# Optimization experiments

Measured on AMD Instinct MI355X. Metric: run time of the kernel, lower is better.

The kernel has to match this reference:

```python
import jax, jax.numpy as jnp
import numpy as np

B, S, D_IN, D_OUT = 4, 2048, 1024, 1024

def setup_inputs() -> dict:
    key = jax.random.key(0)
    kx, kq, kk, kv = jax.random.split(key, 4)
    sc = 1.0 / np.sqrt(D_IN)
    x = jax.random.normal(kx, (B, S, D_IN), dtype=jnp.float32)
    Wq = jax.random.normal(kq, (D_IN, D_OUT), dtype=jnp.float32) * sc
    Wk = jax.random.normal(kk, (D_IN, D_OUT), dtype=jnp.float32) * sc
    Wv = jax.random.normal(kv, (D_IN, D_OUT), dtype=jnp.float32) * sc
    return {"x": x, "Wq": Wq, "Wk": Wk, "Wv": Wv}

def reference(x, Wq, Wk, Wv):
    # x: [B,S,Din]; projections to [B,S,Dout]
    q = jnp.einsum('bsd,de->bse', x, Wq)
    k = jnp.einsum('bsd,de->bse', x, Wk)
    v = jnp.einsum('bsd,de->bse', x, Wv)
    scale = 1.0 / jnp.sqrt(jnp.asarray(q.shape[-1], q.dtype))
    scores = jnp.einsum('bqe,bke->bqk', q, k) * scale  # [B,S,S]
    causal = jnp.tril(jnp.ones((scores.shape[-2], scores.shape[-1]), dtype=bool))
    scores = jnp.where(causal, scores, -jnp.inf)
    attn = jax.nn.softmax(scores, axis=-1)
    # dropout p=0.0 -> identity
    return jnp.einsum('bqk,bke->bqe', attn, v)
```

## Files before the change

### kernel.cpp

```cpp
#include <hip/hip_runtime.h>

#define SEQ 2048
#define DIM 1024

typedef __attribute__((ext_vector_type(8))) __bf16 bf16x8;
typedef __attribute__((ext_vector_type(4))) float f32x4;

typedef __attribute__((address_space(1))) unsigned char gu8_t;
typedef __attribute__((address_space(3))) unsigned char lu8_t;

__device__ __forceinline__ void async_copy16(const void* g, void* l) {
  __builtin_amdgcn_global_load_lds((gu8_t*)g, (lu8_t*)l, 16, 0, 0);
}

__device__ __forceinline__ ushort f2bf(float f) {
  union { float f; unsigned u; } v;
  v.f = f;
  unsigned r = v.u + 0x7FFFu + ((v.u >> 16) & 1u);
  return (ushort)(r >> 16);
}

__global__ void prep(const void* __restrict__ xin, const void* __restrict__ w0,
                     const void* __restrict__ w1, const void* __restrict__ w2,
                     ushort* __restrict__ xb, ushort* __restrict__ wt,
                     int* __restrict__ flag, float* __restrict__ lsum) {
  __shared__ ushort tile[64][68];
  __shared__ int redi[4];
  const int bid = blockIdx.x;
  const int t = threadIdx.x;

  const unsigned* words = (const unsigned*)xin;
  int hits = 0;
#pragma unroll
  for (int i = 0; i < 4; i++) {
    const unsigned wv = words[t * 4 + i];
    const unsigned b = (wv >> 8) & 0x7Fu;
    hits += (b >= 0x3Bu && b <= 0x42u) ? 1 : 0;
  }
#pragma unroll
  for (int o = 32; o > 0; o >>= 1) hits += __shfl_xor(hits, o, 64);
  if ((t & 63) == 0) redi[t >> 6] = hits;
  __syncthreads();
  const int bf = (redi[0] + redi[1] + redi[2] + redi[3] > 512) ? 1 : 0;

  if (bid >= 4864) {
    reinterpret_cast<float4*>(lsum)[(bid - 4864) * 256 + t] =
        make_float4(0.f, 0.f, 0.f, 0.f);
    if (bid == 4864 && t == 0) *flag = bf;
    return;
  }

  if (bid < 4096) {
    const int i = bid * 256 + t;
    if (bf) {
      reinterpret_cast<uint4*>(xb)[i] =
          reinterpret_cast<const uint4*>(xin)[i];
    } else {
      const float4* f = reinterpret_cast<const float4*>(xin);
      const float4 a = f[2 * i], b = f[2 * i + 1];
      ushort4 lo, hi;
      lo.x = f2bf(a.x); lo.y = f2bf(a.y); lo.z = f2bf(a.z); lo.w = f2bf(a.w);
      hi.x = f2bf(b.x); hi.y = f2bf(b.y); hi.z = f2bf(b.z); hi.w = f2bf(b.w);
      reinterpret_cast<ushort4*>(xb)[2 * i] = lo;
      reinterpret_cast<ushort4*>(xb)[2 * i + 1] = hi;
    }
    return;
  }

  const int rem = bid - 4096;
  const int z = rem >> 8;
  const int within = rem & 255;
  const int c0 = (within & 15) * 64, r0 = (within >> 4) * 64;
  const void* in = (z == 0) ? w0 : (z == 1) ? w1 : w2;
  ushort* op = wt + (size_t)z * 1024 * 1024;

  if (bf) {
    const ushort* ip = (const ushort*)in;
#pragma unroll
    for (int i = 0; i < 4; i++) {
      const int lin = i * 256 + t;
      const int r = lin >> 4, c4 = (lin & 15) << 2;
      const ushort4 v = *reinterpret_cast<const ushort4*>(
          ip + (size_t)(r0 + r) * 1024 + c0 + c4);
      tile[r][c4 + 0] = v.x; tile[r][c4 + 1] = v.y;
      tile[r][c4 + 2] = v.z; tile[r][c4 + 3] = v.w;
    }
  } else {
    const float* ip = (const float*)in;
#pragma unroll
    for (int i = 0; i < 4; i++) {
      const int lin = i * 256 + t;
      const int r = lin >> 4, c4 = (lin & 15) << 2;
      const float4 v = *reinterpret_cast<const float4*>(
          ip + (size_t)(r0 + r) * 1024 + c0 + c4);
      tile[r][c4 + 0] = f2bf(v.x); tile[r][c4 + 1] = f2bf(v.y);
      tile[r][c4 + 2] = f2bf(v.z); tile[r][c4 + 3] = f2bf(v.w);
    }
  }
  __syncthreads();
#pragma unroll
  for (int i = 0; i < 4; i++) {
    const int lin = i * 256 + t;
    const int c = lin >> 4, r4 = (lin & 15) << 2;
    ushort4 v;
    v.x = tile[r4 + 0][c]; v.y = tile[r4 + 1][c];
    v.z = tile[r4 + 2][c]; v.w = tile[r4 + 3][c];
    *reinterpret_cast<ushort4*>(op + (size_t)(c0 + c) * 1024 + r0 + r4) = v;
  }
}

template <int EPI>
__global__ __launch_bounds__(512, 2) void gemm8(
    const ushort* __restrict__ P0, const ushort* __restrict__ P1,
    void* __restrict__ Cv, float* __restrict__ lsum) {
  __shared__ ushort sA[2][2][128 * 64];
  __shared__ ushort sB[2][2][128 * 64];

  const ushort* A;
  const ushort* B;
  ushort* C;
  float* ls = nullptr;
  int m0, n0;
  long ldA, ldB, ldC;
  float scale = 1.0f;

  if constexpr (EPI == 0) {
    const int id = blockIdx.x;
    if (id < 256) {
      const int z = id >> 7, r = id & 127;
      m0 = (r >> 2) << 8;
      n0 = (r & 3) << 8;
      A = P0; ldA = 1024;
      B = P1 + (size_t)z * 1024 * 1024; ldB = 1024;
      C = (ushort*)Cv + (size_t)z * 8192 * 1024; ldC = 1024;
      scale = z ? 1.0f : 0.03125f;
    } else {
      const int r = id - 256;
      m0 = (r >> 5) << 8;
      n0 = (r & 31) << 8;
      A = P1 + 2 * 1024 * 1024; ldA = 1024;
      B = P0; ldB = 1024;
      C = (ushort*)Cv + (size_t)16 * 1024 * 1024; ldC = 8192;
    }
  } else {
    const int id = blockIdx.x, z = blockIdx.y;
    int mt = 0;
    while ((mt + 1) * (mt + 2) / 2 <= id) mt++;
    const int nt = id - mt * (mt + 1) / 2;
    m0 = mt << 8;
    n0 = nt << 8;
    A = P0 + (size_t)z * SEQ * DIM; ldA = 1024;
    B = P0 + (size_t)8192 * 1024 + (size_t)z * SEQ * DIM; ldB = 1024;
    C = (ushort*)Cv + (size_t)z * SEQ * SEQ; ldC = 2048;
    ls = lsum + (size_t)z * SEQ;
  }
  const int nT = 16;

  const int tid = threadIdx.x;
  const int lane = tid & 63;
  const int w = tid >> 6;
  const int quad = lane >> 4;
  const int l15 = lane & 15;
  const int ah = w >> 2;
  const int wn = (w & 3) << 6;
  const int bh = wn >> 7;
  const int bo = wn & 64;

  const ushort* aSrc[2][2];
  const ushort* bSrc[2][2];
#pragma unroll
  for (int h = 0; h < 2; h++)
#pragma unroll
    for (int i = 0; i < 2; i++) {
      const int g = i * 512 + tid;
      const int rl = g >> 3;
      const int ck = (g & 7) ^ (rl & 7);
      aSrc[h][i] = A + (size_t)(m0 + h * 128 + rl) * ldA + ck * 8;
      bSrc[h][i] = B + (size_t)(n0 + h * 128 + rl) * ldB + ck * 8;
    }

  auto stageA = [&](int t, int b) {
#pragma unroll
    for (int h = 0; h < 2; h++)
#pragma unroll
      for (int i = 0; i < 2; i++)
        async_copy16(aSrc[h][i] + t * 64, &sA[b][h][(i * 512 + tid) * 8]);
  };
  auto stageB = [&](int t, int b) {
#pragma unroll
    for (int h = 0; h < 2; h++)
#pragma unroll
      for (int i = 0; i < 2; i++)
        async_copy16(bSrc[h][i] + t * 64, &sB[b][h][(i * 512 + tid) * 8]);
  };
  auto rdA = [&](int b, int rbase, int kh) -> bf16x8 {
    const int row = rbase + l15;
    const int ck = ((kh << 2) | quad) ^ (row & 7);
    return *(const bf16x8*)&sA[b][ah][row * 64 + ck * 8];
  };
  auto rdB = [&](int b, int rbase, int kh) -> bf16x8 {
    const int row = rbase + l15;
    const int ck = ((kh << 2) | quad) ^ (row & 7);
    return *(const bf16x8*)&sB[b][bh][row * 64 + ck * 8];
  };

  f32x4 acc[8][4] = {};
  bf16x8 aF[8], bF0[4], bF1[4];

  stageA(0, 0); stageB(0, 0);
  stageA(1, 1); stageB(1, 1);
  asm volatile("s_waitcnt vmcnt(8)" ::: "memory");
  __builtin_amdgcn_s_barrier();

#pragma unroll 1
  for (int t = 0; t < nT; t++) {
    const int b = t & 1;

#pragma unroll
    for (int m = 0; m < 4; m++)
#pragma unroll
      for (int h = 0; h < 2; h++) aF[m * 2 + h] = rdA(b, m * 16, h);
#pragma unroll
    for (int n = 0; n < 2; n++)
#pragma unroll
      for (int h = 0; h < 2; h++) bF0[n * 2 + h] = rdB(b, bo + n * 16, h);
    __builtin_amdgcn_s_barrier();
    __builtin_amdgcn_s_setprio(1);
#pragma unroll
    for (int h = 0; h < 2; h++)
#pragma unroll
      for (int m = 0; m < 4; m++)
#pragma unroll
        for (int n = 0; n < 2; n++)
          acc[m][n] = __builtin_amdgcn_mfma_f32_16x16x32_bf16(
              aF[m * 2 + h], bF0[n * 2 + h], acc[m][n], 0, 0, 0);
    __builtin_amdgcn_s_setprio(0);
    __builtin_amdgcn_s_barrier();

#pragma unroll
    for (int n = 0; n < 2; n++)
#pragma unroll
      for (int h = 0; h < 2; h++)
        bF1[n * 2 + h] = rdB(b, bo + 32 + n * 16, h);
    __builtin_amdgcn_s_barrier();
    __builtin_amdgcn_s_setprio(1);
#pragma unroll
    for (int h = 0; h < 2; h++)
#pragma unroll
      for (int m = 0; m < 4; m++)
#pragma unroll
        for (int n = 0; n < 2; n++)
          acc[m][2 + n] = __builtin_amdgcn_mfma_f32_16x16x32_bf16(
              aF[m * 2 + h], bF1[n * 2 + h], acc[m][2 + n], 0, 0, 0);
    __builtin_amdgcn_s_setprio(0);
    __builtin_amdgcn_s_barrier();

#pragma unroll
    for (int m = 0; m < 4; m++)
#pragma unroll
      for (int h = 0; h < 2; h++) aF[m * 2 + h] = rdA(b, 64 + m * 16, h);
    if (t + 2 < nT) stageB(t + 2, b);
    __builtin_amdgcn_s_barrier();
    __builtin_amdgcn_s_setprio(1);
#pragma unroll
    for (int h = 0; h < 2; h++)
#pragma unroll
      for (int m = 0; m < 4; m++)
#pragma unroll
        for (int n = 0; n < 2; n++)
          acc[4 + m][n] = __builtin_amdgcn_mfma_f32_16x16x32_bf16(
              aF[m * 2 + h], bF0[n * 2 + h], acc[4 + m][n], 0, 0, 0);
    __builtin_amdgcn_s_setprio(0);
    __builtin_amdgcn_s_barrier();

    if (t + 2 < nT) stageA(t + 2, b);
    __builtin_amdgcn_s_setprio(1);
#pragma unroll
    for (int h = 0; h < 2; h++)
#pragma unroll
      for (int m = 0; m < 4; m++)
#pragma unroll
        for (int n = 0; n < 2; n++)
          acc[4 + m][2 + n] = __builtin_amdgcn_mfma_f32_16x16x32_bf16(
              aF[m * 2 + h], bF1[n * 2 + h], acc[4 + m][2 + n], 0, 0, 0);
    __builtin_amdgcn_s_setprio(0);
    if (t + 2 < nT)
      asm volatile("s_waitcnt vmcnt(8)" ::: "memory");
    else
      asm volatile("s_waitcnt vmcnt(0)" ::: "memory");
    __builtin_amdgcn_s_barrier();
  }

  if constexpr (EPI == 0) {
#pragma unroll
    for (int mi = 0; mi < 8; mi++)
#pragma unroll
      for (int ni = 0; ni < 4; ni++)
#pragma unroll
        for (int r = 0; r < 4; r++) {
          const int row = m0 + ah * 128 + mi * 16 + quad * 4 + r;
          const int col = n0 + wn + ni * 16 + l15;
          C[(size_t)row * ldC + col] = f2bf(acc[mi][ni][r] * scale);
        }
  } else {
#pragma unroll
    for (int mi = 0; mi < 8; mi++)
#pragma unroll
      for (int r = 0; r < 4; r++) {
        const int row = m0 + ah * 128 + mi * 16 + quad * 4 + r;
        float partial = 0.0f;
#pragma unroll
        for (int ni = 0; ni < 4; ni++) {
          const int col = n0 + wn + ni * 16 + l15;
          const float ev = (col <= row) ? __expf(acc[mi][ni][r]) : 0.0f;
          C[(size_t)row * ldC + col] = f2bf(ev);
          partial += ev;
        }
#pragma unroll
        for (int o = 1; o < 16; o <<= 1) partial += __shfl_xor(partial, o, 64);
        if (l15 == 0) atomicAdd(&ls[row], partial);
      }
  }
}

template <int EPI, int OUTK, int CK, int SWIZ, int M, int N, int K, long AZ,
          long BZ, long CZ, long BRS>
__global__ __launch_bounds__(256, 4) void gemm_t(
    const ushort* __restrict__ A, const ushort* __restrict__ Bt,
    void* __restrict__ Cv, const int* __restrict__ flag,
    float* __restrict__ lsum, float scale0, float scale1) {
  __shared__ ushort lA[128 * 64];
  __shared__ ushort lB[128 * 64];
  __shared__ float lsh[(EPI == 2) ? 128 : 1];

  constexpr int MT = M / 128;
  const int nT = gridDim.x;
  const int id = blockIdx.y * nT + blockIdx.x;
  const int xcd = id & 7;
  const int loc = id >> 3;
  int nt, mt;
  if constexpr (SWIZ == 1) {
    const int ng = nT >> 3;
    nt = xcd * ng + loc % ng;
    mt = loc / ng;
  } else if constexpr (SWIZ == 2) {
    if (loc <= xcd) { mt = xcd; nt = loc; }
    else { mt = MT - 1 - xcd; nt = loc - xcd - 1; }
  } else if constexpr (SWIZ == 3) {
    nt = xcd;
    mt = loc;
  } else {
    nt = loc % nT;
    mt = xcd + ((loc / nT) << 3);
  }
  const int n0 = nt * 128;
  const int m0 = mt * 128;

  const int z = blockIdx.z;
  const ushort* Ab = A + (size_t)z * AZ;
  const ushort* Bb = Bt + (size_t)z * BZ;

  const int t = threadIdx.x;
  const int lane = t & 63;
  const int w = t >> 6;
  const int wm = (w >> 1) * 64;
  const int wn = (w & 1) * 64;
  const int quad = lane >> 4;
  const int l15 = lane & 15;

  if constexpr (EPI == 2) {
    if (t < 128) lsh[t] = 1.0f / lsum[(size_t)z * M + m0 + t];
  }

  f32x4 acc[4][4] = {};

  const int kEnd = CK ? ((m0 + 128 < K) ? (m0 + 128) : K) : K;

  for (int k0 = 0; k0 < kEnd; k0 += 64) {
    __syncthreads();
#pragma unroll
    for (int g0 = 0; g0 < 1024; g0 += 256) {
      const int g = g0 + t;
      const int r = g >> 3, c = (g & 7) << 3;
      async_copy16(Ab + (size_t)(m0 + r) * K + k0 + c, lA + g * 8);
    }
#pragma unroll
    for (int g0 = 0; g0 < 1024; g0 += 256) {
      const int g = g0 + t;
      const int r = g >> 3, c = (g & 7) << 3;
      async_copy16(Bb + (size_t)(n0 + r) * BRS + k0 + c, lB + g * 8);
    }
    __syncthreads();

#pragma unroll
    for (int h = 0; h < 2; h++) {
      bf16x8 af[4], bfr[4];
#pragma unroll
      for (int mi = 0; mi < 4; mi++)
        af[mi] = *(const bf16x8*)(lA + (wm + mi * 16 + l15) * 64 + h * 32 +
                                  quad * 8);
#pragma unroll
      for (int ni = 0; ni < 4; ni++)
        bfr[ni] = *(const bf16x8*)(lB + (wn + ni * 16 + l15) * 64 + h * 32 +
                                   quad * 8);
#pragma unroll
      for (int mi = 0; mi < 4; mi++)
#pragma unroll
        for (int ni = 0; ni < 4; ni++)
          acc[mi][ni] = __builtin_amdgcn_mfma_f32_16x16x32_bf16(
              af[mi], bfr[ni], acc[mi][ni], 0, 0, 0);
    }
  }

  const size_t zc = (size_t)z * CZ;

  if constexpr (EPI == 1) {
    ushort* C = (ushort*)Cv + zc;
    float* ls = lsum + (size_t)z * M;
#pragma unroll
    for (int mi = 0; mi < 4; mi++)
#pragma unroll
      for (int r = 0; r < 4; r++) {
        const int row = m0 + wm + mi * 16 + quad * 4 + r;
        float partial = 0.0f;
#pragma unroll
        for (int ni = 0; ni < 4; ni++) {
          const int col = n0 + wn + ni * 16 + l15;
          const float ev = (col <= row) ? __expf(acc[mi][ni][r]) : 0.0f;
          C[(size_t)row * N + col] = f2bf(ev);
          partial += ev;
        }
#pragma unroll
        for (int o = 1; o < 16; o <<= 1) partial += __shfl_xor(partial, o, 64);
        if (l15 == 0) atomicAdd(&ls[row], partial);
      }
    return;
  } else {
    const float scale = (z == 0) ? scale0 : scale1;
    const bool storeBf = (OUTK == 1) || (OUTK == 2 && *flag != 0);
#pragma unroll
    for (int mi = 0; mi < 4; mi++)
#pragma unroll
      for (int ni = 0; ni < 4; ni++)
#pragma unroll
        for (int r = 0; r < 4; r++) {
          const int lrow = wm + mi * 16 + quad * 4 + r;
          const int row = m0 + lrow;
          const int col = n0 + wn + ni * 16 + l15;
          const float sc = (EPI == 2) ? lsh[lrow] : scale;
          const float vv = acc[mi][ni][r] * sc;
          if (storeBf) {
            ushort* C = (ushort*)Cv + zc;
            C[(size_t)row * N + col] = f2bf(vv);
          } else {
            float* C = (float*)Cv + zc;
            C[(size_t)row * N + col] = vv;
          }
        }
  }
}

extern "C" void kernel_launch(void* const* d_in, const int* in_sizes, int n_in,
                              void* d_out, int out_size, void* d_ws,
                              size_t ws_size, hipStream_t stream) {
  char* ws = (char*)d_ws;
  const size_t MB = 1024 * 1024;
  int* flag = (int*)ws;
  ushort* wt = (ushort*)(ws + 1 * MB);
  ushort* xb = (ushort*)(ws + 7 * MB);
  ushort* q = (ushort*)(ws + 23 * MB);
  ushort* vt = (ushort*)(ws + 55 * MB);
  ushort* sc = (ushort*)(ws + 71 * MB);
  float* lsum = (float*)(ws + 103 * MB);

  prep<<<dim3(4872), 256, 0, stream>>>(d_in[0], d_in[1], d_in[2], d_in[3], xb,
                                       wt, flag, lsum);

  gemm8<0><<<dim3(384), 512, 0, stream>>>(xb, wt, (void*)q, nullptr);

  gemm8<1><<<dim3(36, 4), 512, 0, stream>>>(q, nullptr, (void*)sc, lsum);

  gemm_t<2, 2, 1, 3, 2048, 1024, 2048, (long)SEQ * SEQ, 2048L,
         (long)SEQ * DIM, 8192L>
      <<<dim3(8, 16, 4), 256, 0, stream>>>(sc, vt, d_out, flag, lsum, 1.0f,
                                           1.0f);
}
```

Baseline: 247.3 us.

## Move V-transpose projection into score kernel launch and coarsen prep blocks

The V^T projection tiles (128 blocks) move out of the QK projection launch and into the causal score-exp launch, which becomes a flat 272-block grid of 144 score tiles plus 128 V tiles. The aim is to fill the idle CUs left by the small triangular score grid and to shorten the projection launch. The prep kernel's x conversion also handles four vectors per thread, cutting its block count. The cost is a mixed-role kernel with per-block branching in the epilogue, and the score blocks' imbalance may now sit alongside the V tiles.

Result: faster. 241.6 us (-2.3%).

```diff
diff --git a/kernel.cpp b/kernel.cpp
--- a/kernel.cpp
+++ b/kernel.cpp
@@ -43,31 +43,34 @@
   __syncthreads();
   const int bf = (redi[0] + redi[1] + redi[2] + redi[3] > 512) ? 1 : 0;
 
-  if (bid >= 4864) {
-    reinterpret_cast<float4*>(lsum)[(bid - 4864) * 256 + t] =
+  if (bid >= 1792) {
+    reinterpret_cast<float4*>(lsum)[(bid - 1792) * 256 + t] =
         make_float4(0.f, 0.f, 0.f, 0.f);
-    if (bid == 4864 && t == 0) *flag = bf;
+    if (bid == 1792 && t == 0) *flag = bf;
     return;
   }
 
-  if (bid < 4096) {
-    const int i = bid * 256 + t;
-    if (bf) {
-      reinterpret_cast<uint4*>(xb)[i] =
-          reinterpret_cast<const uint4*>(xin)[i];
-    } else {
-      const float4* f = reinterpret_cast<const float4*>(xin);
-      const float4 a = f[2 * i], b = f[2 * i + 1];
-      ushort4 lo, hi;
-      lo.x = f2bf(a.x); lo.y = f2bf(a.y); lo.z = f2bf(a.z); lo.w = f2bf(a.w);
-      hi.x = f2bf(b.x); hi.y = f2bf(b.y); hi.z = f2bf(b.z); hi.w = f2bf(b.w);
-      reinterpret_cast<ushort4*>(xb)[2 * i] = lo;
-      reinterpret_cast<ushort4*>(xb)[2 * i + 1] = hi;
+  if (bid < 1024) {
+#pragma unroll
+    for (int j = 0; j < 4; j++) {
+      const int i = bid * 1024 + j * 256 + t;
+      if (bf) {
+        reinterpret_cast<uint4*>(xb)[i] =
+            reinterpret_cast<const uint4*>(xin)[i];
+      } else {
+        const float4* f = reinterpret_cast<const float4*>(xin);
+        const float4 a = f[2 * i], b = f[2 * i + 1];
+        ushort4 lo, hi;
+        lo.x = f2bf(a.x); lo.y = f2bf(a.y); lo.z = f2bf(a.z); lo.w = f2bf(a.w);
+        hi.x = f2bf(b.x); hi.y = f2bf(b.y); hi.z = f2bf(b.z); hi.w = f2bf(b.w);
+        reinterpret_cast<ushort4*>(xb)[2 * i] = lo;
+        reinterpret_cast<ushort4*>(xb)[2 * i + 1] = hi;
+      }
     }
     return;
   }
 
-  const int rem = bid - 4096;
+  const int rem = bid - 1024;
   const int z = rem >> 8;
   const int within = rem & 255;
   const int c0 = (within & 15) * 64, r0 = (within >> 4) * 64;
@@ -109,10 +112,11 @@
   }
 }
 
-template <int EPI>
+template <int MODE>
 __global__ __launch_bounds__(512, 2) void gemm8(
-    const ushort* __restrict__ P0, const ushort* __restrict__ P1,
-    void* __restrict__ Cv, float* __restrict__ lsum) {
+    const ushort* __restrict__ p0, const ushort* __restrict__ p1,
+    const ushort* __restrict__ p2, void* __restrict__ c0,
+    void* __restrict__ c1, float* __restrict__ lsum) {
   __shared__ ushort sA[2][2][128 * 64];
   __shared__ ushort sB[2][2][128 * 64];
 
@@ -123,36 +127,39 @@
   int m0, n0;
   long ldA, ldB, ldC;
   float scale = 1.0f;
-
-  if constexpr (EPI == 0) {
-    const int id = blockIdx.x;
-    if (id < 256) {
-      const int z = id >> 7, r = id & 127;
-      m0 = (r >> 2) << 8;
-      n0 = (r & 3) << 8;
-      A = P0; ldA = 1024;
-      B = P1 + (size_t)z * 1024 * 1024; ldB = 1024;
-      C = (ushort*)Cv + (size_t)z * 8192 * 1024; ldC = 1024;
-      scale = z ? 1.0f : 0.03125f;
+  bool isE = false;
+
+  const int id = blockIdx.x;
+  if constexpr (MODE == 0) {
+    const int z = id >> 7, r = id & 127;
+    m0 = (r >> 2) << 8;
+    n0 = (r & 3) << 8;
+    A = p0; ldA = 1024;
+    B = p1 + (size_t)z * 1024 * 1024; ldB = 1024;
+    C = (ushort*)c0 + (size_t)z * 8192 * 1024; ldC = 1024;
+    scale = z ? 1.0f : 0.03125f;
+  } else {
+    if (id < 144) {
+      isE = true;
+      const int z = id / 36;
+      const int tri = id % 36;
+      int mt = 0;
+      while ((mt + 1) * (mt + 2) / 2 <= tri) mt++;
+      const int nt = tri - mt * (mt + 1) / 2;
+      m0 = mt << 8;
+      n0 = nt << 8;
+      A = p0 + (size_t)z * SEQ * DIM; ldA = 1024;
+      B = p0 + (size_t)8192 * 1024 + (size_t)z * SEQ * DIM; ldB = 1024;
+      C = (ushort*)c0 + (size_t)z * SEQ * SEQ; ldC = 2048;
+      ls = lsum + (size_t)z * SEQ;
     } else {
-      const int r = id - 256;
+      const int r = id - 144;
       m0 = (r >> 5) << 8;
       n0 = (r & 31) << 8;
-      A = P1 + 2 * 1024 * 1024; ldA = 1024;
-      B = P0; ldB = 1024;
-      C = (ushort*)Cv + (size_t)16 * 1024 * 1024; ldC = 8192;
-    }
-  } else {
-    const int id = blockIdx.x, z = blockIdx.y;
-    int mt = 0;
-    while ((mt + 1) * (mt + 2) / 2 <= id) mt++;
-    const int nt = id - mt * (mt + 1) / 2;
-    m0 = mt << 8;
-    n0 = nt << 8;
-    A = P0 + (size_t)z * SEQ * DIM; ldA = 1024;
-    B = P0 + (size_t)8192 * 1024 + (size_t)z * SEQ * DIM; ldB = 1024;
-    C = (ushort*)Cv + (size_t)z * SEQ * SEQ; ldC = 2048;
-    ls = lsum + (size_t)z * SEQ;
+      A = p1 + 2 * 1024 * 1024; ldA = 1024;
+      B = p2; ldB = 1024;
+      C = (ushort*)c1; ldC = 8192;
+    }
   }
   const int nT = 16;
 
@@ -291,18 +298,7 @@
     __builtin_amdgcn_s_barrier();
   }
 
-  if constexpr (EPI == 0) {
-#pragma unroll
-    for (int mi = 0; mi < 8; mi++)
-#pragma unroll
-      for (int ni = 0; ni < 4; ni++)
-#pragma unroll
-        for (int r = 0; r < 4; r++) {
-          const int row = m0 + ah * 128 + mi * 16 + quad * 4 + r;
-          const int col = n0 + wn + ni * 16 + l15;
-          C[(size_t)row * ldC + col] = f2bf(acc[mi][ni][r] * scale);
-        }
-  } else {
+  if (MODE == 1 && isE) {
 #pragma unroll
     for (int mi = 0; mi < 8; mi++)
 #pragma unroll
@@ -320,6 +316,17 @@
         for (int o = 1; o < 16; o <<= 1) partial += __shfl_xor(partial, o, 64);
         if (l15 == 0) atomicAdd(&ls[row], partial);
       }
+  } else {
+#pragma unroll
+    for (int mi = 0; mi < 8; mi++)
+#pragma unroll
+      for (int ni = 0; ni < 4; ni++)
+#pragma unroll
+        for (int r = 0; r < 4; r++) {
+          const int row = m0 + ah * 128 + mi * 16 + quad * 4 + r;
+          const int col = n0 + wn + ni * 16 + l15;
+          C[(size_t)row * ldC + col] = f2bf(acc[mi][ni][r] * scale);
+        }
   }
 }
 
@@ -473,12 +480,14 @@
   ushort* sc = (ushort*)(ws + 71 * MB);
   float* lsum = (float*)(ws + 103 * MB);
 
-  prep<<<dim3(4872), 256, 0, stream>>>(d_in[0], d_in[1], d_in[2], d_in[3], xb,
+  prep<<<dim3(1800), 256, 0, stream>>>(d_in[0], d_in[1], d_in[2], d_in[3], xb,
                                        wt, flag, lsum);
 
-  gemm8<0><<<dim3(384), 512, 0, stream>>>(xb, wt, (void*)q, nullptr);
-
-  gemm8<1><<<dim3(36, 4), 512, 0, stream>>>(q, nullptr, (void*)sc, lsum);
+  gemm8<0><<<dim3(256), 512, 0, stream>>>(xb, wt, nullptr, (void*)q, nullptr,
+                                          nullptr);
+
+  gemm8<1><<<dim3(272), 512, 0, stream>>>(q, wt, xb, (void*)sc, (void*)vt,
+                                          lsum);
 
   gemm_t<2, 2, 1, 3, 2048, 1024, 2048, (long)SEQ * SEQ, 2048L,
          (long)SEQ * DIM, 8192L>
```
